# Kernel optimization log

Measured on AMD Instinct MI355X. Metric: run time of the kernel, lower is better.

Reference implementation:

```python
import jax, jax.numpy as jnp
import numpy as np

B, S, D, H = 4, 2048, 1024, 16
DH = D // H


def setup_inputs() -> dict:
    key = jax.random.key(0)
    ks = jax.random.split(key, 12)
    scale = 1.0 / np.sqrt(D)
    inp = {
        'q': jax.random.normal(ks[0], (B, S, D), jnp.float32),
        'k': jax.random.normal(ks[1], (B, S, D), jnp.float32),
        'v': jax.random.normal(ks[2], (B, S, D), jnp.float32),
        # causal mask, broadcast over batch and heads; masked where mask == 0
        'mask': jnp.tril(jnp.ones((S, S), jnp.int32))[None, None, :, :],
        'wq': jax.random.normal(ks[3], (D, D), jnp.float32) * scale,
        'bq': jnp.zeros((D,), jnp.float32),
        'wk': jax.random.normal(ks[4], (D, D), jnp.float32) * scale,
        'bk': jnp.zeros((D,), jnp.float32),
        'wv': jax.random.normal(ks[5], (D, D), jnp.float32) * scale,
        'bv': jnp.zeros((D,), jnp.float32),
        'wo': jax.random.normal(ks[6], (D, D), jnp.float32) * scale,
        'bo': jnp.zeros((D,), jnp.float32),
    }
    return inp


def _split_heads(x):
    # [B, S, D] -> [B, H, S, DH]
    b, s, _ = x.shape
    return x.reshape(b, s, H, DH).transpose(0, 2, 1, 3)


def reference(q, k, v, mask, wq, bq, wk, bk, wv, bv, wo, bo):
    # torch Linear: y = x @ W.T + b
    qh = _split_heads(q @ wq.T + bq)
    kh = _split_heads(k @ wk.T + bk)
    vh = _split_heads(v @ wv.T + bv)
    attn = jnp.einsum('bhqd,bhkd->bhqk', qh, kh) / np.sqrt(DH)
    attn = jnp.where(mask == 0, jnp.float32(-10000.0), attn)
    attn = jax.nn.softmax(attn, axis=-1)
    out = jnp.einsum('bhqk,bhkd->bhqd', attn, vh)
    out = out.transpose(0, 2, 1, 3).reshape(q.shape[0], q.shape[1], D)
    return out @ wo.T + bo
```

## Files before the change

### kernel.cpp

```cpp
#include <hip/hip_runtime.h>
#include <hip/hip_bf16.h>

typedef __attribute__((ext_vector_type(8))) short short8;
typedef __attribute__((ext_vector_type(4))) float f32x4;
typedef __attribute__((ext_vector_type(16))) float f32x16;
typedef __attribute__((ext_vector_type(4))) unsigned short ushort4v;
typedef __attribute__((ext_vector_type(8))) unsigned short ushort8v;
typedef __attribute__((ext_vector_type(4))) unsigned int uint4v;

#define S_LEN 2048
#define DMODEL 1024
#define NHEAD 16
#define DHEAD 64
#define BATCH 4
#define NEGBIG (-1.0e30f)
#define LOG2E 1.4426950408889634f

__device__ __forceinline__ unsigned short f2bf(float f) {
  unsigned int u = __builtin_bit_cast(unsigned int, f);
  u += 0x7fffu + ((u >> 16) & 1u);
  return (unsigned short)(u >> 16);
}

__device__ __forceinline__ unsigned int pk2bf(float lo, float hi) {
  __hip_bfloat162 t = __float22bfloat162_rn(make_float2(lo, hi));
  unsigned int r;
  __builtin_memcpy(&r, &t, 4);
  return r;
}

__device__ __forceinline__ void gload16(const void* src, void* lds_dst) {
  __builtin_amdgcn_global_load_lds(
      (const __attribute__((address_space(1))) unsigned int*)src,
      (__attribute__((address_space(3))) unsigned int*)lds_dst, 16, 0, 0);
}

__global__ __launch_bounds__(256) void cvt4_kernel(
    const float* __restrict__ i0, const float* __restrict__ i1,
    const float* __restrict__ i2, const float* __restrict__ i3,
    unsigned short* __restrict__ o0, unsigned short* __restrict__ o1,
    unsigned short* __restrict__ o2, unsigned short* __restrict__ o3, int n) {
  const float* in = (blockIdx.y == 0) ? i0 : (blockIdx.y == 1) ? i1 : (blockIdx.y == 2) ? i2 : i3;
  unsigned short* out = (blockIdx.y == 0) ? o0 : (blockIdx.y == 1) ? o1 : (blockIdx.y == 2) ? o2 : o3;
  int idx = blockIdx.x * blockDim.x + threadIdx.x;
  int stride = gridDim.x * blockDim.x;
  for (int j = idx * 8; j < n; j += stride * 8) {
    float4 a = *(const float4*)(in + j);
    float4 b = *(const float4*)(in + j + 4);
    ushort8v r;
    r[0] = f2bf(a.x); r[1] = f2bf(a.y); r[2] = f2bf(a.z); r[3] = f2bf(a.w);
    r[4] = f2bf(b.x); r[5] = f2bf(b.y); r[6] = f2bf(b.z); r[7] = f2bf(b.w);
    *(ushort8v*)(out + j) = r;
  }
}

__global__ __launch_bounds__(256) void qkv_gemm_kernel(
    const float* __restrict__ Aq, const float* __restrict__ Ak, const float* __restrict__ Av,
    const unsigned short* __restrict__ Wq, const unsigned short* __restrict__ Wk,
    const unsigned short* __restrict__ Wv,
    const float* __restrict__ bq, const float* __restrict__ bk, const float* __restrict__ bv,
    unsigned short* __restrict__ oq, unsigned short* __restrict__ ok,
    unsigned short* __restrict__ ov) {
  const int z = blockIdx.z;
  const float* A = (z == 0) ? Aq : (z == 1) ? Ak : Av;
  const unsigned short* W = (z == 0) ? Wq : (z == 1) ? Wk : Wv;
  const float* bias = (z == 0) ? bq : (z == 1) ? bk : bv;
  unsigned short* out = (z == 0) ? oq : (z == 1) ? ok : ov;
  const float oscale = (z == 0) ? 0.125f * LOG2E : 1.0f;
  const int N = DMODEL, K = DMODEL;

  __shared__ char lds[32768];
  const int tid = threadIdx.x;
  const int lane = tid & 63;
  const int wv = tid >> 6;
  const int wr = wv >> 1, wc = wv & 1;
  const int l16 = lane & 15, lg = lane >> 4;

  const int nbx = N >> 7;
  const int swz = (blockIdx.x & 7) * ((int)gridDim.x >> 3) + (blockIdx.x >> 3);
  const int tm = swz / nbx, tn = swz % nbx;

  const char* Wb = (const char*)W;

  const int arow[4] = {(tid >> 3), 32 + (tid >> 3), 64 + (tid >> 3), 96 + (tid >> 3)};
  const int aslot = tid & 7;

  float4 areg[4][2];
#pragma unroll
  for (int j = 0; j < 4; ++j) {
    const float* ap = A + (size_t)(tm * 128 + arow[j]) * K + aslot * 8;
    areg[j][0] = *(const float4*)ap;
    areg[j][1] = *(const float4*)(ap + 4);
  }

  f32x4 acc[4][4] = {};

  for (int k0 = 0; k0 < K; k0 += 64) {
#pragma unroll
    for (int i = 0; i < 4; ++i) {
      int ch = wv * 4 + i;
      int r = ch * 8 + (lane >> 3);
      int cb = ((lane & 7) * 16) ^ ((r & 7) << 4);
      gload16(Wb + ((size_t)(tn * 128 + r) * K + k0) * 2 + cb, lds + 16384 + ch * 1024);
    }
#pragma unroll
    for (int j = 0; j < 4; ++j) {
      uint4v w4;
      w4[0] = pk2bf(areg[j][0].x, areg[j][0].y);
      w4[1] = pk2bf(areg[j][0].z, areg[j][0].w);
      w4[2] = pk2bf(areg[j][1].x, areg[j][1].y);
      w4[3] = pk2bf(areg[j][1].z, areg[j][1].w);
      int r = arow[j];
      *(uint4v*)(lds + r * 128 + ((aslot * 16) ^ ((r & 7) << 4))) = w4;
    }
    __syncthreads();
    if (k0 + 64 < K) {
#pragma unroll
      for (int j = 0; j < 4; ++j) {
        const float* ap = A + (size_t)(tm * 128 + arow[j]) * K + (k0 + 64) + aslot * 8;
        areg[j][0] = *(const float4*)ap;
        areg[j][1] = *(const float4*)(ap + 4);
      }
    }
#pragma unroll
    for (int ks = 0; ks < 2; ++ks) {
      const int cbase = (ks * 32 + lg * 8) * 2;
      short8 af[4], bfr[4];
#pragma unroll
      for (int m = 0; m < 4; ++m) {
        int r = wr * 64 + m * 16 + l16;
        af[m] = *(const short8*)(lds + r * 128 + (cbase ^ ((r & 7) << 4)));
      }
#pragma unroll
      for (int n = 0; n < 4; ++n) {
        int r = wc * 64 + n * 16 + l16;
        bfr[n] = *(const short8*)(lds + 16384 + r * 128 + (cbase ^ ((r & 7) << 4)));
      }
#pragma unroll
      for (int m = 0; m < 4; ++m)
#pragma unroll
        for (int n = 0; n < 4; ++n)
          acc[m][n] = __builtin_amdgcn_mfma_f32_16x16x32_bf16(af[m], bfr[n], acc[m][n], 0, 0, 0);
    }
    asm volatile("s_waitcnt lgkmcnt(0)" ::: "memory");
    __builtin_amdgcn_s_barrier();
    asm volatile("" ::: "memory");
  }

#pragma unroll
  for (int n = 0; n < 4; ++n) {
    int gn = tn * 128 + wc * 64 + n * 16 + l16;
    float bv2 = bias[gn];
    int h = gn >> 6, dh = gn & 63;
#pragma unroll
    for (int m = 0; m < 4; ++m) {
      int gm0 = tm * 128 + wr * 64 + m * 16 + lg * 4;
      f32x4 a = acc[m][n];
      if (z < 2) {
#pragma unroll
        for (int rr = 0; rr < 4; ++rr) {
          int gm = gm0 + rr;
          int b = gm >> 11, s = gm & 2047;
          out[(((size_t)b * NHEAD + h) * S_LEN + s) * DHEAD + dh] = f2bf((a[rr] + bv2) * oscale);
        }
      } else {
        int b = gm0 >> 11, s0 = gm0 & 2047;
        ushort4v pk;
        pk[0] = f2bf(a[0] + bv2); pk[1] = f2bf(a[1] + bv2);
        pk[2] = f2bf(a[2] + bv2); pk[3] = f2bf(a[3] + bv2);
        *(ushort4v*)(out + (((size_t)b * NHEAD + h) * DHEAD + dh) * S_LEN + s0) = pk;
      }
    }
  }
}

__global__ __launch_bounds__(256) void gemm_o_kernel(
    const unsigned short* __restrict__ A, const unsigned short* __restrict__ W,
    const float* __restrict__ bias, float* __restrict__ outp, int M, int N, int K) {
  __shared__ char lds[32768];
  const int tid = threadIdx.x;
  const int lane = tid & 63;
  const int wv = tid >> 6;
  const int wr = wv >> 1, wc = wv & 1;
  const int l16 = lane & 15, lg = lane >> 4;

  const int nbx = N >> 7;
  const int nwg = gridDim.x;
  const int swz = (blockIdx.x & 7) * (nwg >> 3) + (blockIdx.x >> 3);
  const int tm = swz / nbx, tn = swz % nbx;

  const char* Ab = (const char*)A;
  const char* Wb = (const char*)W;

  f32x4 acc[4][4] = {};

  for (int k0 = 0; k0 < K; k0 += 64) {
#pragma unroll
    for (int i = 0; i < 8; ++i) {
      int ch = wv * 8 + i;
      int chl = ch & 15;
      int r = chl * 8 + (lane >> 3);
      int cb = ((lane & 7) * 16) ^ ((r & 7) << 4);
      const char* src = (ch < 16)
          ? Ab + ((size_t)(tm * 128 + r) * K + k0) * 2 + cb
          : Wb + ((size_t)(tn * 128 + r) * K + k0) * 2 + cb;
      gload16(src, lds + ch * 1024);
    }
    __syncthreads();
#pragma unroll
    for (int ks = 0; ks < 2; ++ks) {
      const int cbase = (ks * 32 + lg * 8) * 2;
      short8 af[4], bfr[4];
#pragma unroll
      for (int m = 0; m < 4; ++m) {
        int r = wr * 64 + m * 16 + l16;
        af[m] = *(const short8*)(lds + r * 128 + (cbase ^ ((r & 7) << 4)));
      }
#pragma unroll
      for (int n = 0; n < 4; ++n) {
        int r = wc * 64 + n * 16 + l16;
        bfr[n] = *(const short8*)(lds + 16384 + r * 128 + (cbase ^ ((r & 7) << 4)));
      }
#pragma unroll
      for (int m = 0; m < 4; ++m)
#pragma unroll
        for (int n = 0; n < 4; ++n)
          acc[m][n] = __builtin_amdgcn_mfma_f32_16x16x32_bf16(af[m], bfr[n], acc[m][n], 0, 0, 0);
    }
    __syncthreads();
  }

#pragma unroll
  for (int n = 0; n < 4; ++n) {
    int gn = tn * 128 + wc * 64 + n * 16 + l16;
    float bv = bias[gn];
#pragma unroll
    for (int m = 0; m < 4; ++m) {
      int gm0 = tm * 128 + wr * 64 + m * 16 + lg * 4;
      f32x4 a = acc[m][n];
#pragma unroll
      for (int rr = 0; rr < 4; ++rr)
        outp[(size_t)(gm0 + rr) * N + gn] = a[rr] + bv;
    }
  }
}

__global__ __launch_bounds__(256) void attn_kernel(
    const unsigned short* __restrict__ qh, const unsigned short* __restrict__ kh,
    const unsigned short* __restrict__ vt, unsigned short* __restrict__ aout) {
  __shared__ char lds[32768];
  const int tid = threadIdx.x;
  const int lane = tid & 63;
  const int w = tid >> 6;
  const int l31 = lane & 31;
  const int l5 = lane >> 5;
  const int bh = blockIdx.x;
  const int b = bh >> 4, h = bh & 15;

  const char* kbase = (const char*)(kh + (size_t)bh * S_LEN * DHEAD);
  const char* vbase = (const char*)(vt + (size_t)bh * S_LEN * DHEAD);
  const unsigned short* qbase = qh + (size_t)bh * S_LEN * DHEAD;

  const int la = lane >> 3, lb = lane & 7;

  const int qb = 15 - (int)blockIdx.y;
  const int q0 = qb * 128;
  const int wq0 = q0 + w * 32;
  const int qg = wq0 + l31;
  const int nt = qb * 2 + 2;

  short8 qf[4];
#pragma unroll
  for (int f = 0; f < 4; ++f)
    qf[f] = *(const short8*)(qbase + (size_t)qg * DHEAD + f * 16 + l5 * 8);

  f32x16 oa[2] = {};
  float mrun = NEGBIG, lr = 0.f;

#pragma unroll
  for (int i = 0; i < 2; ++i) {
    int ch = w * 2 + i;
    int r = ch * 8 + la;
    int cb = (lb * 16) ^ ((r & 7) << 4);
    gload16(kbase + (size_t)r * 128 + cb, lds + ch * 1024 + lane * 16);
    gload16(vbase + (size_t)r * 4096 + cb, lds + 8192 + ch * 1024 + lane * 16);
  }
  __syncthreads();
  int cur = 0;

  for (int t = 0; t < nt; ++t) {
    const int kv0 = t * 64;
    if (t + 1 < nt) {
      char* nb = lds + (cur ^ 1) * 16384;
#pragma unroll
      for (int i = 0; i < 2; ++i) {
        int ch = w * 2 + i;
        int r = ch * 8 + la;
        int cb = (lb * 16) ^ ((r & 7) << 4);
        gload16(kbase + (size_t)(kv0 + 64 + r) * 128 + cb, nb + ch * 1024 + lane * 16);
        gload16(vbase + (size_t)r * 4096 + (size_t)(kv0 + 64) * 2 + cb,
                nb + 8192 + ch * 1024 + lane * 16);
      }
    }
    if (kv0 <= wq0 + 31) {
      const char* ldk = lds + cur * 16384;
      const char* ldv = ldk + 8192;

      f32x16 sa[2] = {};
      __builtin_amdgcn_s_setprio(1);
#pragma unroll
      for (int kb2 = 0; kb2 < 2; ++kb2) {
        const int kr = kb2 * 32 + l31;
        const char* rowp = ldk + kr * 128;
        const int sw = (kr & 7) << 4;
#pragma unroll
        for (int f = 0; f < 4; ++f) {
          short8 kf = *(const short8*)(rowp + ((f * 32 + l5 * 16) ^ sw));
          sa[kb2] = __builtin_amdgcn_mfma_f32_32x32x16_bf16(kf, qf[f], sa[kb2], 0, 0, 0);
        }
      }
      __builtin_amdgcn_s_setprio(0);

      if (kv0 + 63 > wq0) {
#pragma unroll
        for (int kb2 = 0; kb2 < 2; ++kb2)
#pragma unroll
          for (int r = 0; r < 16; ++r) {
            int kgl = kv0 + kb2 * 32 + (r & 3) + 8 * (r >> 2) + 4 * l5;
            if (kgl > qg) sa[kb2][r] = NEGBIG;
          }
      }

      float pm = sa[0][0];
#pragma unroll
      for (int kb2 = 0; kb2 < 2; ++kb2)
#pragma unroll
        for (int r = 0; r < 16; ++r) pm = fmaxf(pm, sa[kb2][r]);
      pm = fmaxf(pm, __shfl_xor(pm, 32));

      if (!__all(pm <= mrun + 8.f)) {
        float mN = fmaxf(mrun, pm);
        float sc = __builtin_amdgcn_exp2f(mrun - mN);
        mrun = mN;
        lr *= sc;
        oa[0] *= sc;
        oa[1] *= sc;
      }

      float rs = 0.f;
      short8 pfrag[4];
#pragma unroll
      for (int kb2 = 0; kb2 < 2; ++kb2) {
        unsigned int wpk[8];
#pragma unroll
        for (int i = 0; i < 8; ++i) {
          float p0 = __builtin_amdgcn_exp2f(sa[kb2][2 * i] - mrun);
          float p1 = __builtin_amdgcn_exp2f(sa[kb2][2 * i + 1] - mrun);
          rs += p0 + p1;
          wpk[i] = pk2bf(p0, p1);
        }
#pragma unroll
        for (int g = 0; g < 2; ++g) {
          unsigned int o0 = l5 ? wpk[4 * g + 2] : wpk[4 * g];
          unsigned int o1 = l5 ? wpk[4 * g + 3] : wpk[4 * g + 1];
          unsigned int s0 = l5 ? wpk[4 * g] : wpk[4 * g + 2];
          unsigned int s1 = l5 ? wpk[4 * g + 1] : wpk[4 * g + 3];
          unsigned int r0 = (unsigned int)__shfl_xor((int)s0, 32);
          unsigned int r1 = (unsigned int)__shfl_xor((int)s1, 32);
          uint4v fw;
          fw[0] = l5 ? r0 : o0;
          fw[1] = l5 ? r1 : o1;
          fw[2] = l5 ? o0 : r0;
          fw[3] = l5 ? o1 : r1;
          pfrag[kb2 * 2 + g] = __builtin_bit_cast(short8, fw);
        }
      }
      rs += __shfl_xor(rs, 32);
      lr += rs;

      __builtin_amdgcn_s_setprio(1);
#pragma unroll
      for (int db = 0; db < 2; ++db) {
        const int vr = db * 32 + l31;
        const char* rowp = ldv + vr * 128;
        const int sw = (vr & 7) << 4;
#pragma unroll
        for (int f = 0; f < 4; ++f) {
          short8 vf = *(const short8*)(rowp + ((f * 32 + l5 * 16) ^ sw));
          oa[db] = __builtin_amdgcn_mfma_f32_32x32x16_bf16(vf, pfrag[f], oa[db], 0, 0, 0);
        }
      }
      __builtin_amdgcn_s_setprio(0);
    }
    __syncthreads();
    cur ^= 1;
  }

  float rl = 1.0f / lr;
  unsigned short* obase = aout + ((size_t)(b * S_LEN + qg)) * DMODEL + h * DHEAD;
#pragma unroll
  for (int db = 0; db < 2; ++db)
#pragma unroll
    for (int rq = 0; rq < 4; ++rq) {
      ushort4v pk;
#pragma unroll
      for (int j = 0; j < 4; ++j)
        pk[j] = f2bf(oa[db][rq * 4 + j] * rl);
      *(ushort4v*)(obase + db * 32 + 8 * rq + 4 * l5) = pk;
    }
}

extern "C" void kernel_launch(void* const* d_in, const int* in_sizes, int n_in,
                              void* d_out, int out_size, void* d_ws, size_t ws_size,
                              hipStream_t stream) {
  (void)in_sizes; (void)n_in; (void)out_size; (void)ws_size;
  const float* q  = (const float*)d_in[0];
  const float* k  = (const float*)d_in[1];
  const float* v  = (const float*)d_in[2];
  const float* wq = (const float*)d_in[4];
  const float* bq = (const float*)d_in[5];
  const float* wk = (const float*)d_in[6];
  const float* bk = (const float*)d_in[7];
  const float* wv = (const float*)d_in[8];
  const float* bv = (const float*)d_in[9];
  const float* wo = (const float*)d_in[10];
  const float* bo = (const float*)d_in[11];

  const size_t NACT = (size_t)BATCH * S_LEN * DMODEL;
  const size_t NW = (size_t)DMODEL * DMODEL;
  unsigned short* wqb = (unsigned short*)d_ws;
  unsigned short* wkb = wqb + NW;
  unsigned short* wvb = wkb + NW;
  unsigned short* wob = wvb + NW;
  unsigned short* qhb = wob + NW;
  unsigned short* khb = qhb + NACT;
  unsigned short* vtb = khb + NACT;
  unsigned short* aout = vtb + NACT;

  dim3 blk(256);
  cvt4_kernel<<<dim3(512, 4), blk, 0, stream>>>(wq, wk, wv, wo, wqb, wkb, wvb, wob, (int)NW);

  const int M = BATCH * S_LEN, N = DMODEL, K = DMODEL;
  const int grid = (M / 128) * (N / 128);
  qkv_gemm_kernel<<<dim3(grid, 1, 3), blk, 0, stream>>>(
      q, k, v, wqb, wkb, wvb, bq, bk, bv, qhb, khb, vtb);

  attn_kernel<<<dim3(64, 16), blk, 0, stream>>>(qhb, khb, vtb, aout);

  gemm_o_kernel<<<grid, blk, 0, stream>>>(aout, wob, bo, (float*)d_out, M, N, K);
}
```

Measured before the change: 182.5 us.

## Double-buffer weight tiles in QKV GEMM to overlap loads with MFMA

The QKV projection GEMM now keeps two LDS buffers for the bf16 weight tile, which grows LDS from 32KB to 48KB. The next tile's async global-to-LDS weight load and fp32 activation load are issued before the current tile's MFMA work. The aim is to hide global memory latency behind compute instead of waiting on each tile before computing. The costs are an extra barrier per iteration and higher LDS use, which may reduce occupancy.

```diff
diff --git a/kernel.cpp b/kernel.cpp
--- a/kernel.cpp
+++ b/kernel.cpp
@@ -69,7 +69,7 @@
   const float oscale = (z == 0) ? 0.125f * LOG2E : 1.0f;
   const int N = DMODEL, K = DMODEL;
 
-  __shared__ char lds[32768];
+  __shared__ char lds[49152];
   const int tid = threadIdx.x;
   const int lane = tid & 63;
   const int wv = tid >> 6;
@@ -86,23 +86,26 @@
   const int aslot = tid & 7;
 
   float4 areg[4][2];
-#pragma unroll
-  for (int j = 0; j < 4; ++j) {
-    const float* ap = A + (size_t)(tm * 128 + arow[j]) * K + aslot * 8;
-    areg[j][0] = *(const float4*)ap;
-    areg[j][1] = *(const float4*)(ap + 4);
-  }
-
-  f32x4 acc[4][4] = {};
-
-  for (int k0 = 0; k0 < K; k0 += 64) {
+
+  auto loadA = [&](int k0) {
+#pragma unroll
+    for (int j = 0; j < 4; ++j) {
+      const float* ap = A + (size_t)(tm * 128 + arow[j]) * K + k0 + aslot * 8;
+      areg[j][0] = *(const float4*)ap;
+      areg[j][1] = *(const float4*)(ap + 4);
+    }
+  };
+  auto stageB = [&](int k0, int buf) {
 #pragma unroll
     for (int i = 0; i < 4; ++i) {
       int ch = wv * 4 + i;
       int r = ch * 8 + (lane >> 3);
       int cb = ((lane & 7) * 16) ^ ((r & 7) << 4);
-      gload16(Wb + ((size_t)(tn * 128 + r) * K + k0) * 2 + cb, lds + 16384 + ch * 1024);
-    }
+      gload16(Wb + ((size_t)(tn * 128 + r) * K + k0) * 2 + cb,
+              lds + 16384 + buf * 16384 + ch * 1024);
+    }
+  };
+  auto cvtWriteA = [&]() {
 #pragma unroll
     for (int j = 0; j < 4; ++j) {
       uint4v w4;
@@ -113,15 +116,23 @@
       int r = arow[j];
       *(uint4v*)(lds + r * 128 + ((aslot * 16) ^ ((r & 7) << 4))) = w4;
     }
-    __syncthreads();
-    if (k0 + 64 < K) {
-#pragma unroll
-      for (int j = 0; j < 4; ++j) {
-        const float* ap = A + (size_t)(tm * 128 + arow[j]) * K + (k0 + 64) + aslot * 8;
-        areg[j][0] = *(const float4*)ap;
-        areg[j][1] = *(const float4*)(ap + 4);
-      }
-    }
+  };
+
+  f32x4 acc[4][4] = {};
+
+  loadA(0);
+  stageB(0, 0);
+  cvtWriteA();
+  __syncthreads();
+
+  int cur = 0;
+  for (int k0 = 0; k0 < K; k0 += 64) {
+    const bool more = (k0 + 64 < K);
+    if (more) {
+      loadA(k0 + 64);
+      stageB(k0 + 64, cur ^ 1);
+    }
+    const char* Bb = lds + 16384 + cur * 16384;
 #pragma unroll
     for (int ks = 0; ks < 2; ++ks) {
       const int cbase = (ks * 32 + lg * 8) * 2;
@@ -134,7 +145,7 @@
 #pragma unroll
       for (int n = 0; n < 4; ++n) {
         int r = wc * 64 + n * 16 + l16;
-        bfr[n] = *(const short8*)(lds + 16384 + r * 128 + (cbase ^ ((r & 7) << 4)));
+        bfr[n] = *(const short8*)(Bb + r * 128 + (cbase ^ ((r & 7) << 4)));
       }
 #pragma unroll
       for (int m = 0; m < 4; ++m)
@@ -142,9 +153,14 @@
         for (int n = 0; n < 4; ++n)
           acc[m][n] = __builtin_amdgcn_mfma_f32_16x16x32_bf16(af[m], bfr[n], acc[m][n], 0, 0, 0);
     }
-    asm volatile("s_waitcnt lgkmcnt(0)" ::: "memory");
-    __builtin_amdgcn_s_barrier();
-    asm volatile("" ::: "memory");
+    if (more) {
+      asm volatile("s_waitcnt lgkmcnt(0)" ::: "memory");
+      __builtin_amdgcn_s_barrier();
+      asm volatile("" ::: "memory");
+      cvtWriteA();
+      __syncthreads();
+    }
+    cur ^= 1;
   }
 
 #pragma unroll
```

Result: slower. 283.2 us (+55.2%).
